# Kernel optimization log

Measured on AMD Instinct MI355X. Metric: run time of the kernel, lower is better.

Reference implementation:

```python
import jax, jax.numpy as jnp
import numpy as np
from jax import lax

D_MODEL = 768
EXPAND = 2
D_INNER = D_MODEL * EXPAND  # 1536
N_STATE = 16
DT_RANK = D_INNER // 16  # 96
K_CONV = 4
B, L = 2, 1024


def setup_inputs() -> dict:
    key = jax.random.key(0)
    ks = jax.random.split(key, 20)
    s = lambda i, shape, scale=0.02: jax.random.normal(ks[i], shape, dtype=jnp.float32) * scale
    # dt_proj bias init (inverse softplus of dt in [0.001, 0.1])
    def dt_bias(k):
        dt = jnp.exp(jax.random.uniform(k, (D_INNER,)) * (np.log(0.1) - np.log(0.001)) + np.log(0.001))
        return dt + jnp.log(-jnp.expm1(-dt))
    A_log = jnp.log(jnp.arange(1, N_STATE + 1, dtype=jnp.float32))[None, :] * jnp.ones((D_INNER, 1), jnp.float32)
    inp = {
        "u": jax.random.normal(ks[0], (B, L, D_MODEL), dtype=jnp.float32),
        "norm_w": jnp.ones((D_MODEL,), jnp.float32),
        "norm_b": jnp.zeros((D_MODEL,), jnp.float32),
        "fwd_in_w": s(1, (2 * D_INNER, D_MODEL)),
        "fwd_conv_w": s(2, (D_INNER, 1, K_CONV), 0.1),
        "fwd_conv_b": jnp.zeros((D_INNER,), jnp.float32),
        "fwd_A_log": A_log,
        "fwd_xproj_w": s(3, (DT_RANK + 2 * N_STATE, D_INNER)),
        "fwd_dt_w": s(4, (D_INNER, DT_RANK)),
        "fwd_dt_b": dt_bias(ks[5]),
        "fwd_D": jnp.ones((D_INNER,), jnp.float32),
        "bwd_in_w": s(6, (2 * D_INNER, D_MODEL)),
        "bwd_conv_w": s(7, (D_INNER, 1, K_CONV), 0.1),
        "bwd_conv_b": jnp.zeros((D_INNER,), jnp.float32),
        "bwd_A_log": A_log,
        "bwd_xproj_w": s(8, (DT_RANK + 2 * N_STATE, D_INNER)),
        "bwd_dt_w": s(9, (D_INNER, DT_RANK)),
        "bwd_dt_b": dt_bias(ks[10]),
        "bwd_D": jnp.ones((D_INNER,), jnp.float32),
        "out_w": s(11, (D_MODEL, 2 * D_INNER)),
    }
    return inp


def _layernorm(x, w, b, eps=1e-5):
    mu = jnp.mean(x, axis=-1, keepdims=True)
    var = jnp.mean(jnp.square(x - mu), axis=-1, keepdims=True)
    return (x - mu) * lax.rsqrt(var + eps) * w + b


def _dw_causal_conv(x, w, b):
    # x: (B, L, D); torch Conv1d(pad=k-1, groups=D) then trim to L == left-pad causal conv
    xc = jnp.transpose(x, (0, 2, 1))  # (B, D, L)
    y = lax.conv_general_dilated(xc, w, window_strides=(1,),
                                 padding=[(K_CONV - 1, 0)],
                                 feature_group_count=D_INNER,
                                 dimension_numbers=('NCH', 'OIH', 'NCH'))
    return jnp.transpose(y + b[None, :, None], (0, 2, 1))


def _ssm(x, A_log, xproj_w, dt_w, dt_b, Dp):
    # x: (B, L, D)
    x_dbl = x @ xproj_w.T  # (B, L, dt_rank + 2N)
    dt_raw = x_dbl[..., :DT_RANK]
    B_sel = x_dbl[..., DT_RANK:DT_RANK + N_STATE]   # (B, L, N)
    C_sel = x_dbl[..., DT_RANK + N_STATE:]           # (B, L, N)
    dt = jax.nn.softplus(dt_raw @ dt_w.T + dt_b)      # (B, L, D)
    A = -jnp.exp(A_log)                               # (D, N)
    A_bar = jnp.exp(dt[..., None] * A)                # (B, L, D, N)
    Bu = (dt * x)[..., None] * B_sel[:, :, None, :]   # (B, L, D, N)
    # linear recurrence h_t = A_bar_t * h_{t-1} + Bu_t via associative scan
    def combine(c1, c2):
        a1, b1 = c1
        a2, b2 = c2
        return a1 * a2, a2 * b1 + b2
    _, h = lax.associative_scan(combine, (A_bar, Bu), axis=1)
    y = jnp.einsum('bldn,bln->bld', h, C_sel)
    return y + x * Dp


def _branch(u, in_w, conv_w, conv_b, A_log, xproj_w, dt_w, dt_b, Dp, reverse):
    if reverse:
        u = u[:, ::-1]
    xz = u @ in_w.T
    x, z = xz[..., :D_INNER], xz[..., D_INNER:]
    x = jax.nn.silu(_dw_causal_conv(x, conv_w, conv_b))
    x = _ssm(x, A_log, xproj_w, dt_w, dt_b, Dp)
    x = x * jax.nn.silu(z)
    if reverse:
        x = x[:, ::-1]
    return x


def reference(u, norm_w, norm_b,
              fwd_in_w, fwd_conv_w, fwd_conv_b, fwd_A_log, fwd_xproj_w, fwd_dt_w, fwd_dt_b, fwd_D,
              bwd_in_w, bwd_conv_w, bwd_conv_b, bwd_A_log, bwd_xproj_w, bwd_dt_w, bwd_dt_b, bwd_D,
              out_w):
    residual = u
    un = _layernorm(u, norm_w, norm_b)
    x_fwd = _branch(un, fwd_in_w, fwd_conv_w, fwd_conv_b, fwd_A_log, fwd_xproj_w, fwd_dt_w, fwd_dt_b, fwd_D, False)
    x_bwd = _branch(un, bwd_in_w, bwd_conv_w, bwd_conv_b, bwd_A_log, bwd_xproj_w, bwd_dt_w, bwd_dt_b, bwd_D, True)
    x = jnp.concatenate([x_fwd, x_bwd], axis=-1) @ out_w.T
    return x + residual
```

## Files before the change

kernel.cpp:

```cpp
#include <hip/hip_runtime.h>
#include <hip/hip_bf16.h>

#define D_MODEL 768
#define D_INNER 1536
#define N_STATE 16
#define DT_RANK 96
#define KCONV   4
#define Bv      2
#define Lv      1024
#define MROWS   (Bv*Lv)
#define CH      128
#define G       (Lv/CH)
#define PADL    68

typedef __attribute__((ext_vector_type(8))) short bf16x8;
typedef __attribute__((ext_vector_type(4))) float f32x4;

__device__ __forceinline__ void gll16(const void* g, void* l) {
    __builtin_amdgcn_global_load_lds(
        (const __attribute__((address_space(1))) void*)g,
        (__attribute__((address_space(3))) void*)l, 16, 0, 0);
}

__device__ __forceinline__ unsigned short f2bf(float f) {
    unsigned u = __builtin_bit_cast(unsigned, f);
    u += 0x7fffu + ((u >> 16) & 1u);
    return (unsigned short)(u >> 16);
}

template<int CTRL>
__device__ __forceinline__ float dpp_ror_add(float v) {
    int vi = __builtin_bit_cast(int, v);
    int mv = __builtin_amdgcn_update_dpp(vi, vi, CTRL, 0xf, 0xf, true);
    return v + __builtin_bit_cast(float, mv);
}

__global__ __launch_bounds__(256)
void ln_kernel(const float* __restrict__ u, const float* __restrict__ w,
               const float* __restrict__ bvec, unsigned short* __restrict__ o)
{
    int row = blockIdx.x;
    const float* x = u + (size_t)row * D_MODEL;
    int t = threadIdx.x;
    float v0 = x[t], v1 = x[t + 256], v2 = x[t + 512];
    float s  = v0 + v1 + v2;
    float s2 = v0*v0 + v1*v1 + v2*v2;
    for (int off = 32; off; off >>= 1) {
        s  += __shfl_down(s, off);
        s2 += __shfl_down(s2, off);
    }
    __shared__ float rs[4], rs2[4];
    __shared__ float mu_s, rstd_s;
    int wid = t >> 6, lane = t & 63;
    if (lane == 0) { rs[wid] = s; rs2[wid] = s2; }
    __syncthreads();
    if (t == 0) {
        float S  = rs[0] + rs[1] + rs[2] + rs[3];
        float S2 = rs2[0] + rs2[1] + rs2[2] + rs2[3];
        float mu = S / (float)D_MODEL;
        float var = S2 / (float)D_MODEL - mu * mu;
        mu_s = mu;
        rstd_s = rsqrtf(var + 1e-5f);
    }
    __syncthreads();
    float mu = mu_s, r = rstd_s;
    unsigned short* orow = o + (size_t)row * D_MODEL;
    orow[t]       = f2bf((v0 - mu) * r * w[t]       + bvec[t]);
    orow[t + 256] = f2bf((v1 - mu) * r * w[t + 256] + bvec[t + 256]);
    orow[t + 512] = f2bf((v2 - mu) * r * w[t + 512] + bvec[t + 512]);
}

__global__ __launch_bounds__(256)
void f2b(const float* __restrict__ in, unsigned short* __restrict__ o, int n4)
{
    int i = blockIdx.x * 256 + threadIdx.x;
    if (i < n4) {
        float4 v = ((const float4*)in)[i];
        ushort4 r;
        r.x = f2bf(v.x); r.y = f2bf(v.y); r.z = f2bf(v.z); r.w = f2bf(v.w);
        ((ushort4*)o)[i] = r;
    }
}

__global__ __launch_bounds__(256)
void gemm_mfma(const unsigned short* __restrict__ A, int lda, int revA, int Lr,
               const unsigned short* __restrict__ W,
               const float* __restrict__ bias, int act,
               const float* __restrict__ res,
               float* __restrict__ C,
               int M, int N, int K)
{
    __shared__ unsigned short As[128 * 32];
    __shared__ unsigned short Bs[128 * 32];
    const int tid = threadIdx.x;
    const int m0 = blockIdx.y * 128, n0 = blockIdx.x * 128;
    const int lane = tid & 63;
    const int w  = tid >> 6;
    const int wr = w >> 1, wc = w & 1;
    const int lm = lane & 15, lk = lane >> 4;

    const int srow = tid >> 2;
    const int skq  = (tid & 3) * 8;
    int arow0 = m0 + srow, arow1 = m0 + srow + 64;
    if (revA) {
        arow0 = (arow0 / Lr) * Lr + (Lr - 1 - arow0 % Lr);
        arow1 = (arow1 / Lr) * Lr + (Lr - 1 - arow1 % Lr);
    }
    const unsigned short* a0 = A + (size_t)arow0 * lda + skq;
    const unsigned short* a1 = A + (size_t)arow1 * lda + skq;
    const unsigned short* w0 = W + (size_t)(n0 + srow) * K + skq;
    const unsigned short* w1 = W + (size_t)(n0 + srow + 64) * K + skq;

    f32x4 acc[4][4] = {};

    for (int k0 = 0; k0 < K; k0 += 32) {
        __syncthreads();
        gll16(a0 + k0, &As[tid * 8]);
        gll16(a1 + k0, &As[2048 + tid * 8]);
        gll16(w0 + k0, &Bs[tid * 8]);
        gll16(w1 + k0, &Bs[2048 + tid * 8]);
        __syncthreads();

        bf16x8 af[4], bfr[4];
        #pragma unroll
        for (int i = 0; i < 4; i++) {
            af[i]  = *(const bf16x8*)&As[(wr * 64 + i * 16 + lm) * 32 + lk * 8];
            bfr[i] = *(const bf16x8*)&Bs[(wc * 64 + i * 16 + lm) * 32 + lk * 8];
        }
        #pragma unroll
        for (int i = 0; i < 4; i++)
            #pragma unroll
            for (int j = 0; j < 4; j++)
                acc[i][j] = __builtin_amdgcn_mfma_f32_16x16x32_bf16(af[i], bfr[j], acc[i][j], 0, 0, 0);
    }

    #pragma unroll
    for (int i = 0; i < 4; i++) {
        #pragma unroll
        for (int j = 0; j < 4; j++) {
            int row = m0 + wr * 64 + i * 16 + lk * 4;
            int col = n0 + wc * 64 + j * 16 + lm;
            #pragma unroll
            for (int r = 0; r < 4; r++) {
                float v = acc[i][j][r];
                if (bias) v += bias[col];
                if (act == 2) v = (v > 20.f) ? v : log1pf(__expf(v));
                if (res)  v += res[(size_t)(row + r) * N + col];
                C[(size_t)(row + r) * N + col] = v;
            }
        }
    }
}

__global__ __launch_bounds__(256)
void conv_silu(const float* __restrict__ xz, const float* __restrict__ w,
               const float* __restrict__ bias, float* __restrict__ xo,
               unsigned short* __restrict__ xbf)
{
    int t  = blockIdx.x * 256 + threadIdx.x;
    int d  = t % D_INNER;
    int lc = (t / D_INNER) % (Lv / 8);
    int b  = t / (D_INNER * (Lv / 8));
    int l0 = lc * 8;
    const float* src = xz + (size_t)b * Lv * (2 * D_INNER) + d;
    float w0 = w[d*4], w1 = w[d*4+1], w2 = w[d*4+2], w3 = w[d*4+3];
    float bb = bias[d];
    float v[11];
    #pragma unroll
    for (int j = 0; j < 11; j++) {
        int l = l0 - 3 + j;
        v[j] = (l >= 0) ? src[(size_t)l * (2 * D_INNER)] : 0.f;
    }
    size_t base = ((size_t)b * Lv + l0) * D_INNER + d;
    #pragma unroll
    for (int j = 0; j < 8; j++) {
        float a = bb + w0*v[j] + w1*v[j+1] + w2*v[j+2] + w3*v[j+3];
        a = a / (1.f + __expf(-a));
        xo[base + (size_t)j * D_INNER] = a;
        xbf[base + (size_t)j * D_INNER] = f2bf(a);
    }
}

__global__ __launch_bounds__(128, 6)
void scan1(const float* __restrict__ xF, const float* __restrict__ dtF,
           const float* __restrict__ xdF, const float* __restrict__ AlF,
           const float* __restrict__ xB, const float* __restrict__ dtB,
           const float* __restrict__ xdB, const float* __restrict__ AlB,
           float* __restrict__ h_end, float* __restrict__ Send)
{
    const int br = blockIdx.z;
    const int bb = blockIdx.y >> 3, g = blockIdx.y & 7;
    const int d0 = blockIdx.x * 8;

    const float* x    = br ? xB  : xF;
    const float* dt   = br ? dtB : dtF;
    const float* xd   = br ? xdB : xdF;
    const float* Alog = br ? AlB : AlF;

    __shared__ float xs [2][8][PADL];
    __shared__ float dls[2][8][PADL];
    __shared__ float Bss[2][16][PADL];

    const int t = threadIdx.x;
    const int n = t & 15, dloc = t >> 4;

    const float* xg  = x  + ((size_t)bb * Lv + g * CH) * D_INNER + d0;
    const float* dtg = dt + ((size_t)bb * Lv + g * CH) * D_INNER + d0;
    const float* bcg = xd + ((size_t)bb * Lv + g * CH) * 128;

    const int sl = t >> 1, sdq = (t & 1) * 4;
    const int bl0 = t >> 2,         bq0 = (t & 3) * 4;
    const int bl1 = (t + 128) >> 2, bq1 = ((t + 128) & 3) * 4;

    f32x4 rx, rdt, rb0, rb1;

    #define LOADG1(c) do {                                                       \
        int l0_ = (c) * 64;                                                      \
        rx  = *(const f32x4*)(xg  + (size_t)(l0_ + sl) * D_INNER + sdq);         \
        rdt = *(const f32x4*)(dtg + (size_t)(l0_ + sl) * D_INNER + sdq);         \
        rb0 = *(const f32x4*)(bcg + (size_t)(l0_ + bl0) * 128 + DT_RANK + bq0);  \
        rb1 = *(const f32x4*)(bcg + (size_t)(l0_ + bl1) * 128 + DT_RANK + bq1);  \
    } while (0)

    #define WRITEL1(p) do {                                                     \
        _Pragma("unroll")                                                       \
        for (int j = 0; j < 4; j++) {                                           \
            xs [p][sdq+j][sl] = rx[j];                                          \
            dls[p][sdq+j][sl] = rdt[j];                                         \
            Bss[p][bq0+j][bl0] = rb0[j];                                        \
            Bss[p][bq1+j][bl1] = rb1[j];                                        \
        }                                                                       \
    } while (0)

    const float An = -__expf(Alog[(d0 + dloc) * N_STATE + n]);
    float h = 0.f, srun = 0.f;

    LOADG1(0);
    WRITEL1(0);
    __syncthreads();

    for (int c = 0; c < 2; ++c) {
        const int p = c;
        if (c == 0) LOADG1(1);

        #pragma unroll
        for (int gg = 0; gg < 16; ++gg) {
            f32x4 xv  = *(const f32x4*)&xs [p][dloc][gg*4];
            f32x4 dtv = *(const f32x4*)&dls[p][dloc][gg*4];
            f32x4 bv  = *(const f32x4*)&Bss[p][n][gg*4];
            #pragma unroll
            for (int j = 0; j < 4; ++j) {
                float ab = __expf(dtv[j] * An);
                h = fmaf(ab, h, dtv[j] * xv[j] * bv[j]);
                srun += dtv[j];
            }
        }
        if (c == 0) { WRITEL1(1); }
        __syncthreads();
    }
    h_end[(((size_t)(br*Bv + bb) * G + g) * D_INNER + d0 + dloc) * 16 + n] = h;
    if (n == 0)
        Send[((size_t)(br*Bv + bb) * G + g) * D_INNER + d0 + dloc] = srun;
    #undef LOADG1
    #undef WRITEL1
}

__global__ __launch_bounds__(256)
void scan2(const float* __restrict__ Send,
           const float* __restrict__ AlF, const float* __restrict__ AlB,
           const float* __restrict__ h_end, float* __restrict__ h0buf)
{
    int idx = blockIdx.x * 256 + threadIdx.x;
    int n = idx & 15;
    int rest = idx >> 4;
    int d  = rest % D_INNER;
    int bbr = rest / D_INNER;
    int bb = bbr & 1, br = bbr >> 1;

    const float* Alog = br ? AlB : AlF;
    float An = -__expf(Alog[d * N_STATE + n]);

    float h0 = 0.f;
    #pragma unroll
    for (int g = 0; g < G; ++g) {
        size_t base = (((size_t)(br*Bv + bb) * G + g) * D_INNER + d) * 16 + n;
        h0buf[base] = h0;
        float Se = Send[((size_t)(br*Bv + bb) * G + g) * D_INNER + d];
        h0 = __expf(An * Se) * h0 + h_end[base];
    }
}

__global__ __launch_bounds__(128, 4)
void scan3(const float* __restrict__ xF, const float* __restrict__ dtF,
           const float* __restrict__ xdF, const float* __restrict__ xzF,
           const float* __restrict__ AlF, const float* __restrict__ DFp,
           const float* __restrict__ xB, const float* __restrict__ dtB,
           const float* __restrict__ xdB, const float* __restrict__ xzB,
           const float* __restrict__ AlB, const float* __restrict__ DBp,
           const float* __restrict__ h0buf, unsigned short* __restrict__ ycat)
{
    const int br = blockIdx.z;
    const int bb = blockIdx.y >> 3, g = blockIdx.y & 7;
    const int d0 = blockIdx.x * 8;

    const float* x    = br ? xB  : xF;
    const float* dt   = br ? dtB : dtF;
    const float* xd   = br ? xdB : xdF;
    const float* xz   = br ? xzB : xzF;
    const float* Alog = br ? AlB : AlF;
    const float* Dp   = br ? DBp : DFp;

    __shared__ float xs [2][8][PADL];
    __shared__ float dls[2][8][PADL];
    __shared__ float zs [2][8][PADL];
    __shared__ float Bss[2][16][PADL];
    __shared__ float Css[2][16][PADL];

    const int t = threadIdx.x;
    const int n = t & 15, dloc = t >> 4;

    const float* xg  = x  + ((size_t)bb * Lv + g * CH) * D_INNER + d0;
    const float* dtg = dt + ((size_t)bb * Lv + g * CH) * D_INNER + d0;
    const float* zg  = xz + ((size_t)bb * Lv + g * CH) * (2*D_INNER) + D_INNER + d0;
    const float* bcg = xd + ((size_t)bb * Lv + g * CH) * 128;

    const int sl = t >> 1, sdq = (t & 1) * 4;
    const int bl0 = t >> 2,         bq0 = (t & 3) * 4;
    const int bl1 = (t + 128) >> 2, bq1 = ((t + 128) & 3) * 4;

    f32x4 rx, rdt, rz, rb0, rb1, rc0, rc1;

    #define LOADG3(c) do {                                                       \
        int l0_ = (c) * 64;                                                      \
        rx  = *(const f32x4*)(xg  + (size_t)(l0_ + sl) * D_INNER + sdq);         \
        rdt = *(const f32x4*)(dtg + (size_t)(l0_ + sl) * D_INNER + sdq);         \
        rz  = *(const f32x4*)(zg  + (size_t)(l0_ + sl) * (2*D_INNER) + sdq);     \
        rb0 = *(const f32x4*)(bcg + (size_t)(l0_ + bl0) * 128 + DT_RANK           + bq0); \
        rb1 = *(const f32x4*)(bcg + (size_t)(l0_ + bl1) * 128 + DT_RANK           + bq1); \
        rc0 = *(const f32x4*)(bcg + (size_t)(l0_ + bl0) * 128 + DT_RANK + N_STATE + bq0); \
        rc1 = *(const f32x4*)(bcg + (size_t)(l0_ + bl1) * 128 + DT_RANK + N_STATE + bq1); \
    } while (0)

    #define WRITEL3(p) do {                                                     \
        _Pragma("unroll")                                                       \
        for (int j = 0; j < 4; j++) {                                           \
            xs [p][sdq+j][sl] = rx[j];                                          \
            dls[p][sdq+j][sl] = rdt[j];                                         \
            zs [p][sdq+j][sl] = rz[j];                                          \
            Bss[p][bq0+j][bl0] = rb0[j];                                        \
            Bss[p][bq1+j][bl1] = rb1[j];                                        \
            Css[p][bq0+j][bl0] = rc0[j];                                        \
            Css[p][bq1+j][bl1] = rc1[j];                                        \
        }                                                                       \
    } while (0)

    const float An = -__expf(Alog[(d0 + dloc) * N_STATE + n]);
    const float Dd = Dp[d0 + dloc];
    float h = h0buf[(((size_t)(br*Bv + bb) * G + g) * D_INNER + d0 + dloc) * 16 + n];

    LOADG3(0);
    WRITEL3(0);
    __syncthreads();

    for (int c = 0; c < 2; ++c) {
        const int p = c;
        if (c == 0) LOADG3(1);

        float yq[4] = {};
        #pragma unroll
        for (int gg = 0; gg < 16; ++gg) {
            f32x4 xv  = *(const f32x4*)&xs [p][dloc][gg*4];
            f32x4 dtv = *(const f32x4*)&dls[p][dloc][gg*4];
            f32x4 zv  = *(const f32x4*)&zs [p][dloc][gg*4];
            f32x4 bv  = *(const f32x4*)&Bss[p][n][gg*4];
            f32x4 cv  = *(const f32x4*)&Css[p][n][gg*4];
            #pragma unroll
            for (int j = 0; j < 4; ++j) {
                const int l = gg * 4 + j;
                float ab = __expf(dtv[j] * An);
                h = fmaf(ab, h, dtv[j] * xv[j] * bv[j]);
                float contrib = h * cv[j];
                contrib = dpp_ror_add<0x121>(contrib);
                contrib = dpp_ror_add<0x122>(contrib);
                contrib = dpp_ror_add<0x124>(contrib);
                contrib = dpp_ror_add<0x128>(contrib);
                float y = (contrib + xv[j] * Dd)
                        * (zv[j] * __builtin_amdgcn_rcpf(1.f + __expf(-zv[j])));
                if ((l & 15) == n) yq[l >> 4] = y;
            }
        }
        if (c == 0) { WRITEL3(1); }

        #pragma unroll
        for (int q = 0; q < 4; ++q) {
            int gl = g * CH + c * 64 + q * 16 + n;
            int lo = br ? (Lv - 1 - gl) : gl;
            ycat[((size_t)bb * Lv + lo) * (2*D_INNER) + br * D_INNER + d0 + dloc] = f2bf(yq[q]);
        }
        __syncthreads();
    }
    #undef LOADG3
    #undef WRITEL3
}

extern "C" void kernel_launch(void* const* d_in, const int* in_sizes, int n_in,
                              void* d_out, int out_size, void* d_ws, size_t ws_size,
                              hipStream_t stream)
{
    (void)in_sizes; (void)n_in; (void)out_size; (void)ws_size;
    const float* u        = (const float*)d_in[0];
    const float* norm_w   = (const float*)d_in[1];
    const float* norm_b   = (const float*)d_in[2];
    const float* f_in_w   = (const float*)d_in[3];
    const float* f_conv_w = (const float*)d_in[4];
    const float* f_conv_b = (const float*)d_in[5];
    const float* f_Alog   = (const float*)d_in[6];
    const float* f_xproj  = (const float*)d_in[7];
    const float* f_dt_w   = (const float*)d_in[8];
    const float* f_dt_b   = (const float*)d_in[9];
    const float* f_D      = (const float*)d_in[10];
    const float* b_in_w   = (const float*)d_in[11];
    const float* b_conv_w = (const float*)d_in[12];
    const float* b_conv_b = (const float*)d_in[13];
    const float* b_Alog   = (const float*)d_in[14];
    const float* b_xproj  = (const float*)d_in[15];
    const float* b_dt_w   = (const float*)d_in[16];
    const float* b_dt_b   = (const float*)d_in[17];
    const float* b_D      = (const float*)d_in[18];
    const float* out_w    = (const float*)d_in[19];
    float* out = (float*)d_out;

    float* p = (float*)d_ws;
    unsigned short* un_bf = (unsigned short*)p;  p += (size_t)MROWS * D_MODEL;
    float* xz_f   = p;  p += (size_t)MROWS * 2 * D_INNER;
    float* xz_b   = p;  p += (size_t)MROWS * 2 * D_INNER;
    float* x_f    = p;  p += (size_t)MROWS * D_INNER;
    float* x_b    = p;  p += (size_t)MROWS * D_INNER;
    unsigned short* xbf_f = (unsigned short*)p;  p += (size_t)MROWS * D_INNER / 2;
    unsigned short* xbf_b = (unsigned short*)p;  p += (size_t)MROWS * D_INNER / 2;
    float* xdbl_f = p;  p += (size_t)MROWS * 128;
    float* xdbl_b = p;  p += (size_t)MROWS * 128;
    float* dt_f   = p;  p += (size_t)MROWS * D_INNER;
    float* dt_b_  = p;  p += (size_t)MROWS * D_INNER;
    unsigned short* yc_bf = (unsigned short*)p;  p += (size_t)MROWS * D_INNER;
    unsigned short* fw_bf = (unsigned short*)p;  p += (size_t)D_INNER * D_MODEL;
    unsigned short* bw_bf = (unsigned short*)p;  p += (size_t)D_INNER * D_MODEL;
    unsigned short* xwf_bf = (unsigned short*)p; p += (size_t)64 * D_INNER;
    unsigned short* xwb_bf = (unsigned short*)p; p += (size_t)64 * D_INNER;
    unsigned short* ow_bf = (unsigned short*)p;  p += (size_t)D_MODEL * D_INNER;
    float* h_end  = p;  p += (size_t)2 * Bv * G * D_INNER * N_STATE;
    float* h0buf  = p;  p += (size_t)2 * Bv * G * D_INNER * N_STATE;
    float* Send   = p;  p += (size_t)2 * Bv * G * D_INNER;
    unsigned short* xdbf_f = (unsigned short*)p; p += (size_t)MROWS * 128 / 2;
    unsigned short* xdbf_b = (unsigned short*)p; p += (size_t)MROWS * 128 / 2;
    unsigned short* dtwf_bf = (unsigned short*)p; p += (size_t)D_INNER * DT_RANK / 2;
    unsigned short* dtwb_bf = (unsigned short*)p; p += (size_t)D_INNER * DT_RANK / 2;

    ln_kernel<<<MROWS, 256, 0, stream>>>(u, norm_w, norm_b, un_bf);

    f2b<<<(2*D_INNER*D_MODEL/4 + 255)/256, 256, 0, stream>>>(f_in_w, fw_bf, 2*D_INNER*D_MODEL/4);
    f2b<<<(2*D_INNER*D_MODEL/4 + 255)/256, 256, 0, stream>>>(b_in_w, bw_bf, 2*D_INNER*D_MODEL/4);
    f2b<<<(128*D_INNER/4 + 255)/256, 256, 0, stream>>>(f_xproj, xwf_bf, 128*D_INNER/4);
    f2b<<<(128*D_INNER/4 + 255)/256, 256, 0, stream>>>(b_xproj, xwb_bf, 128*D_INNER/4);
    f2b<<<(D_MODEL*2*D_INNER/4 + 255)/256, 256, 0, stream>>>(out_w, ow_bf, D_MODEL*2*D_INNER/4);
    f2b<<<(D_INNER*DT_RANK/4 + 255)/256, 256, 0, stream>>>(f_dt_w, dtwf_bf, D_INNER*DT_RANK/4);
    f2b<<<(D_INNER*DT_RANK/4 + 255)/256, 256, 0, stream>>>(b_dt_w, dtwb_bf, D_INNER*DT_RANK/4);

    gemm_mfma<<<dim3(2*D_INNER/128, MROWS/128), 256, 0, stream>>>(
        un_bf, D_MODEL, 0, Lv, fw_bf, nullptr, 0, nullptr, xz_f, MROWS, 2*D_INNER, D_MODEL);
    gemm_mfma<<<dim3(2*D_INNER/128, MROWS/128), 256, 0, stream>>>(
        un_bf, D_MODEL, 1, Lv, bw_bf, nullptr, 0, nullptr, xz_b, MROWS, 2*D_INNER, D_MODEL);

    int convBlocks = (Bv * (Lv/8) * D_INNER) / 256;
    conv_silu<<<convBlocks, 256, 0, stream>>>(xz_f, f_conv_w, f_conv_b, x_f, xbf_f);
    conv_silu<<<convBlocks, 256, 0, stream>>>(xz_b, b_conv_w, b_conv_b, x_b, xbf_b);

    gemm_mfma<<<dim3(1, MROWS/128), 256, 0, stream>>>(
        xbf_f, D_INNER, 0, Lv, xwf_bf, nullptr, 0, nullptr, xdbl_f, MROWS, 128, D_INNER);
    gemm_mfma<<<dim3(1, MROWS/128), 256, 0, stream>>>(
        xbf_b, D_INNER, 0, Lv, xwb_bf, nullptr, 0, nullptr, xdbl_b, MROWS, 128, D_INNER);

    f2b<<<(MROWS*128/4 + 255)/256, 256, 0, stream>>>(xdbl_f, xdbf_f, MROWS*128/4);
    f2b<<<(MROWS*128/4 + 255)/256, 256, 0, stream>>>(xdbl_b, xdbf_b, MROWS*128/4);
    gemm_mfma<<<dim3(D_INNER/128, MROWS/128), 256, 0, stream>>>(
        xdbf_f, 128, 0, Lv, dtwf_bf, f_dt_b, 2, nullptr, dt_f, MROWS, D_INNER, DT_RANK);
    gemm_mfma<<<dim3(D_INNER/128, MROWS/128), 256, 0, stream>>>(
        xdbf_b, 128, 0, Lv, dtwb_bf, b_dt_b, 2, nullptr, dt_b_, MROWS, D_INNER, DT_RANK);

    scan1<<<dim3(D_INNER/8, Bv*G, 2), 128, 0, stream>>>(
        x_f, dt_f, xdbl_f, f_Alog,
        x_b, dt_b_, xdbl_b, b_Alog, h_end, Send);
    scan2<<<(2*Bv*D_INNER*N_STATE)/256, 256, 0, stream>>>(
        Send, f_Alog, b_Alog, h_end, h0buf);
    scan3<<<dim3(D_INNER/8, Bv*G, 2), 128, 0, stream>>>(
        x_f, dt_f, xdbl_f, xz_f, f_Alog, f_D,
        x_b, dt_b_, xdbl_b, xz_b, b_Alog, b_D, h0buf, yc_bf);

    gemm_mfma<<<dim3(D_MODEL/128, MROWS/128), 256, 0, stream>>>(
        yc_bf, 2*D_INNER, 0, Lv, ow_bf, nullptr, 0, u, out, MROWS, D_MODEL, 2*D_INNER);
}
```

Baseline: 570.8 us.

## Split in-proj output, fuse silu(z) into GEMM epilogue, use bf16 x/z in scans

The in-projection GEMM epilogue now writes the x half as fp32 and the z half as bf16 with silu already applied. The conv kernel then reads a compact x buffer and no longer writes an fp32 copy. Both scan kernels read x and silu(z) as bf16 from the existing bf16 buffers and keep them in smaller shared-memory arrays. This cuts global memory traffic and scan shared-memory footprint (scan1 occupancy hint raised to 7), at the cost of bf16 rounding of x and z inside the recurrence.

Measured after the change: 610.5 us. 1.07x slower.

```diff
diff --git a/kernel.cpp b/kernel.cpp
--- a/kernel.cpp
+++ b/kernel.cpp
@@ -26,6 +26,9 @@
     unsigned u = __builtin_bit_cast(unsigned, f);
     u += 0x7fffu + ((u >> 16) & 1u);
     return (unsigned short)(u >> 16);
+}
+__device__ __forceinline__ float b2f(unsigned short s) {
+    return __builtin_bit_cast(float, (unsigned)s << 16);
 }
 
 template<int CTRL>
@@ -87,7 +90,7 @@
                const unsigned short* __restrict__ W,
                const float* __restrict__ bias, int act,
                const float* __restrict__ res,
-               float* __restrict__ C,
+               float* __restrict__ C, unsigned short* __restrict__ Cz,
                int M, int N, int K)
 {
     __shared__ unsigned short As[128 * 32];
@@ -143,48 +146,55 @@
             #pragma unroll
             for (int r = 0; r < 4; r++) {
                 float v = acc[i][j][r];
-                if (bias) v += bias[col];
-                if (act == 2) v = (v > 20.f) ? v : log1pf(__expf(v));
-                if (res)  v += res[(size_t)(row + r) * N + col];
-                C[(size_t)(row + r) * N + col] = v;
+                if (act == 3) {
+                    if (col < D_INNER) {
+                        C[(size_t)(row + r) * D_INNER + col] = v;
+                    } else {
+                        float sv = v * __builtin_amdgcn_rcpf(1.f + __expf(-v));
+                        Cz[(size_t)(row + r) * D_INNER + (col - D_INNER)] = f2bf(sv);
+                    }
+                } else {
+                    if (bias) v += bias[col];
+                    if (act == 2) v = (v > 20.f) ? v : log1pf(__expf(v));
+                    if (res)  v += res[(size_t)(row + r) * N + col];
+                    C[(size_t)(row + r) * N + col] = v;
+                }
             }
         }
     }
 }
 
 __global__ __launch_bounds__(256)
-void conv_silu(const float* __restrict__ xz, const float* __restrict__ w,
-               const float* __restrict__ bias, float* __restrict__ xo,
-               unsigned short* __restrict__ xbf)
+void conv_silu(const float* __restrict__ xzx, const float* __restrict__ w,
+               const float* __restrict__ bias, unsigned short* __restrict__ xbf)
 {
     int t  = blockIdx.x * 256 + threadIdx.x;
     int d  = t % D_INNER;
     int lc = (t / D_INNER) % (Lv / 8);
     int b  = t / (D_INNER * (Lv / 8));
     int l0 = lc * 8;
-    const float* src = xz + (size_t)b * Lv * (2 * D_INNER) + d;
+    const float* src = xzx + (size_t)b * Lv * D_INNER + d;
     float w0 = w[d*4], w1 = w[d*4+1], w2 = w[d*4+2], w3 = w[d*4+3];
     float bb = bias[d];
     float v[11];
     #pragma unroll
     for (int j = 0; j < 11; j++) {
         int l = l0 - 3 + j;
-        v[j] = (l >= 0) ? src[(size_t)l * (2 * D_INNER)] : 0.f;
+        v[j] = (l >= 0) ? src[(size_t)l * D_INNER] : 0.f;
     }
     size_t base = ((size_t)b * Lv + l0) * D_INNER + d;
     #pragma unroll
     for (int j = 0; j < 8; j++) {
         float a = bb + w0*v[j] + w1*v[j+1] + w2*v[j+2] + w3*v[j+3];
         a = a / (1.f + __expf(-a));
-        xo[base + (size_t)j * D_INNER] = a;
         xbf[base + (size_t)j * D_INNER] = f2bf(a);
     }
 }
 
-__global__ __launch_bounds__(128, 6)
-void scan1(const float* __restrict__ xF, const float* __restrict__ dtF,
+__global__ __launch_bounds__(128, 7)
+void scan1(const unsigned short* __restrict__ xF, const float* __restrict__ dtF,
            const float* __restrict__ xdF, const float* __restrict__ AlF,
-           const float* __restrict__ xB, const float* __restrict__ dtB,
+           const unsigned short* __restrict__ xB, const float* __restrict__ dtB,
            const float* __restrict__ xdB, const float* __restrict__ AlB,
            float* __restrict__ h_end, float* __restrict__ Send)
 {
@@ -192,19 +202,19 @@
     const int bb = blockIdx.y >> 3, g = blockIdx.y & 7;
     const int d0 = blockIdx.x * 8;
 
-    const float* x    = br ? xB  : xF;
+    const unsigned short* x = br ? xB  : xF;
     const float* dt   = br ? dtB : dtF;
     const float* xd   = br ? xdB : xdF;
     const float* Alog = br ? AlB : AlF;
 
-    __shared__ float xs [2][8][PADL];
+    __shared__ unsigned short xsh[2][8][PADL];
     __shared__ float dls[2][8][PADL];
     __shared__ float Bss[2][16][PADL];
 
     const int t = threadIdx.x;
     const int n = t & 15, dloc = t >> 4;
 
-    const float* xg  = x  + ((size_t)bb * Lv + g * CH) * D_INNER + d0;
+    const unsigned short* xg = x + ((size_t)bb * Lv + g * CH) * D_INNER + d0;
     const float* dtg = dt + ((size_t)bb * Lv + g * CH) * D_INNER + d0;
     const float* bcg = xd + ((size_t)bb * Lv + g * CH) * 128;
 
@@ -212,20 +222,21 @@
     const int bl0 = t >> 2,         bq0 = (t & 3) * 4;
     const int bl1 = (t + 128) >> 2, bq1 = ((t + 128) & 3) * 4;
 
-    f32x4 rx, rdt, rb0, rb1;
+    ushort4 rxu; f32x4 rdt, rb0, rb1;
 
     #define LOADG1(c) do {                                                       \
         int l0_ = (c) * 64;                                                      \
-        rx  = *(const f32x4*)(xg  + (size_t)(l0_ + sl) * D_INNER + sdq);         \
+        rxu = *(const ushort4*)(xg + (size_t)(l0_ + sl) * D_INNER + sdq);        \
         rdt = *(const f32x4*)(dtg + (size_t)(l0_ + sl) * D_INNER + sdq);         \
         rb0 = *(const f32x4*)(bcg + (size_t)(l0_ + bl0) * 128 + DT_RANK + bq0);  \
         rb1 = *(const f32x4*)(bcg + (size_t)(l0_ + bl1) * 128 + DT_RANK + bq1);  \
     } while (0)
 
     #define WRITEL1(p) do {                                                     \
+        xsh[p][sdq+0][sl] = rxu.x; xsh[p][sdq+1][sl] = rxu.y;                   \
+        xsh[p][sdq+2][sl] = rxu.z; xsh[p][sdq+3][sl] = rxu.w;                   \
         _Pragma("unroll")                                                       \
         for (int j = 0; j < 4; j++) {                                           \
-            xs [p][sdq+j][sl] = rx[j];                                          \
             dls[p][sdq+j][sl] = rdt[j];                                         \
             Bss[p][bq0+j][bl0] = rb0[j];                                        \
             Bss[p][bq1+j][bl1] = rb1[j];                                        \
@@ -245,13 +256,14 @@
 
         #pragma unroll
         for (int gg = 0; gg < 16; ++gg) {
-            f32x4 xv  = *(const f32x4*)&xs [p][dloc][gg*4];
+            ushort4 xv4 = *(const ushort4*)&xsh[p][dloc][gg*4];
             f32x4 dtv = *(const f32x4*)&dls[p][dloc][gg*4];
             f32x4 bv  = *(const f32x4*)&Bss[p][n][gg*4];
+            float xf[4] = { b2f(xv4.x), b2f(xv4.y), b2f(xv4.z), b2f(xv4.w) };
             #pragma unroll
             for (int j = 0; j < 4; ++j) {
                 float ab = __expf(dtv[j] * An);
-                h = fmaf(ab, h, dtv[j] * xv[j] * bv[j]);
+                h = fmaf(ab, h, dtv[j] * xf[j] * bv[j]);
                 srun += dtv[j];
             }
         }
@@ -291,11 +303,11 @@
 }
 
 __global__ __launch_bounds__(128, 4)
-void scan3(const float* __restrict__ xF, const float* __restrict__ dtF,
-           const float* __restrict__ xdF, const float* __restrict__ xzF,
+void scan3(const unsigned short* __restrict__ xF, const float* __restrict__ dtF,
+           const float* __restrict__ xdF, const unsigned short* __restrict__ zF,
            const float* __restrict__ AlF, const float* __restrict__ DFp,
-           const float* __restrict__ xB, const float* __restrict__ dtB,
-           const float* __restrict__ xdB, const float* __restrict__ xzB,
+           const unsigned short* __restrict__ xB, const float* __restrict__ dtB,
+           const float* __restrict__ xdB, const unsigned short* __restrict__ zB,
            const float* __restrict__ AlB, const float* __restrict__ DBp,
            const float* __restrict__ h0buf, unsigned short* __restrict__ ycat)
 {
@@ -303,38 +315,38 @@
     const int bb = blockIdx.y >> 3, g = blockIdx.y & 7;
     const int d0 = blockIdx.x * 8;
 
-    const float* x    = br ? xB  : xF;
+    const unsigned short* x = br ? xB : xF;
     const float* dt   = br ? dtB : dtF;
     const float* xd   = br ? xdB : xdF;
-    const float* xz   = br ? xzB : xzF;
+    const unsigned short* z = br ? zB : zF;
     const float* Alog = br ? AlB : AlF;
     const float* Dp   = br ? DBp : DFp;
 
-    __shared__ float xs [2][8][PADL];
+    __shared__ unsigned short xsh[2][8][PADL];
     __shared__ float dls[2][8][PADL];
-    __shared__ float zs [2][8][PADL];
+    __shared__ unsigned short zsh[2][8][PADL];
     __shared__ float Bss[2][16][PADL];
     __shared__ float Css[2][16][PADL];
 
     const int t = threadIdx.x;
     const int n = t & 15, dloc = t >> 4;
 
-    const float* xg  = x  + ((size_t)bb * Lv + g * CH) * D_INNER + d0;
+    const unsigned short* xg = x + ((size_t)bb * Lv + g * CH) * D_INNER + d0;
     const float* dtg = dt + ((size_t)bb * Lv + g * CH) * D_INNER + d0;
-    const float* zg  = xz + ((size_t)bb * Lv + g * CH) * (2*D_INNER) + D_INNER + d0;
+    const unsigned short* zg = z + ((size_t)bb * Lv + g * CH) * D_INNER + d0;
     const float* bcg = xd + ((size_t)bb * Lv + g * CH) * 128;
 
     const int sl = t >> 1, sdq = (t & 1) * 4;
     const int bl0 = t >> 2,         bq0 = (t & 3) * 4;
     const int bl1 = (t + 128) >> 2, bq1 = ((t + 128) & 3) * 4;
 
-    f32x4 rx, rdt, rz, rb0, rb1, rc0, rc1;
+    ushort4 rxu, rzu; f32x4 rdt, rb0, rb1, rc0, rc1;
 
     #define LOADG3(c) do {                                                       \
         int l0_ = (c) * 64;                                                      \
-        rx  = *(const f32x4*)(xg  + (size_t)(l0_ + sl) * D_INNER + sdq);         \
+        rxu = *(const ushort4*)(xg + (size_t)(l0_ + sl) * D_INNER + sdq);        \
         rdt = *(const f32x4*)(dtg + (size_t)(l0_ + sl) * D_INNER + sdq);         \
-        rz  = *(const f32x4*)(zg  + (size_t)(l0_ + sl) * (2*D_INNER) + sdq);     \
+        rzu = *(const ushort4*)(zg + (size_t)(l0_ + sl) * D_INNER + sdq);        \
         rb0 = *(const f32x4*)(bcg + (size_t)(l0_ + bl0) * 128 + DT_RANK           + bq0); \
         rb1 = *(const f32x4*)(bcg + (size_t)(l0_ + bl1) * 128 + DT_RANK           + bq1); \
         rc0 = *(const f32x4*)(bcg + (size_t)(l0_ + bl0) * 128 + DT_RANK + N_STATE + bq0); \
@@ -342,11 +354,13 @@
     } while (0)
 
     #define WRITEL3(p) do {                                                     \
+        xsh[p][sdq+0][sl] = rxu.x; xsh[p][sdq+1][sl] = rxu.y;                   \
+        xsh[p][sdq+2][sl] = rxu.z; xsh[p][sdq+3][sl] = rxu.w;                   \
+        zsh[p][sdq+0][sl] = rzu.x; zsh[p][sdq+1][sl] = rzu.y;                   \
+        zsh[p][sdq+2][sl] = rzu.z; zsh[p][sdq+3][sl] = rzu.w;                   \
         _Pragma("unroll")                                                       \
         for (int j = 0; j < 4; j++) {                                           \
-            xs [p][sdq+j][sl] = rx[j];                                          \
             dls[p][sdq+j][sl] = rdt[j];                                         \
-            zs [p][sdq+j][sl] = rz[j];                                          \
             Bss[p][bq0+j][bl0] = rb0[j];                                        \
             Bss[p][bq1+j][bl1] = rb1[j];                                        \
             Css[p][bq0+j][bl0] = rc0[j];                                        \
@@ -369,23 +383,24 @@
         float yq[4] = {};
         #pragma unroll
         for (int gg = 0; gg < 16; ++gg) {
-            f32x4 xv  = *(const f32x4*)&xs [p][dloc][gg*4];
+            ushort4 xv4 = *(const ushort4*)&xsh[p][dloc][gg*4];
             f32x4 dtv = *(const f32x4*)&dls[p][dloc][gg*4];
-            f32x4 zv  = *(const f32x4*)&zs [p][dloc][gg*4];
+            ushort4 zv4 = *(const ushort4*)&zsh[p][dloc][gg*4];
             f32x4 bv  = *(const f32x4*)&Bss[p][n][gg*4];
             f32x4 cv  = *(const f32x4*)&Css[p][n][gg*4];
+            float xf[4] = { b2f(xv4.x), b2f(xv4.y), b2f(xv4.z), b2f(xv4.w) };
+            float zf[4] = { b2f(zv4.x), b2f(zv4.y), b2f(zv4.z), b2f(zv4.w) };
             #pragma unroll
             for (int j = 0; j < 4; ++j) {
                 const int l = gg * 4 + j;
                 float ab = __expf(dtv[j] * An);
-                h = fmaf(ab, h, dtv[j] * xv[j] * bv[j]);
+                h = fmaf(ab, h, dtv[j] * xf[j] * bv[j]);
                 float contrib = h * cv[j];
                 contrib = dpp_ror_add<0x121>(contrib);
                 contrib = dpp_ror_add<0x122>(contrib);
                 contrib = dpp_ror_add<0x124>(contrib);
                 contrib = dpp_ror_add<0x128>(contrib);
-                float y = (contrib + xv[j] * Dd)
-                        * (zv[j] * __builtin_amdgcn_rcpf(1.f + __expf(-zv[j])));
+                float y = (contrib + xf[j] * Dd) * zf[j];
                 if ((l & 15) == n) yq[l >> 4] = y;
             }
         }
@@ -432,10 +447,10 @@
 
     float* p = (float*)d_ws;
     unsigned short* un_bf = (unsigned short*)p;  p += (size_t)MROWS * D_MODEL;
-    float* xz_f   = p;  p += (size_t)MROWS * 2 * D_INNER;
-    float* xz_b   = p;  p += (size_t)MROWS * 2 * D_INNER;
-    float* x_f    = p;  p += (size_t)MROWS * D_INNER;
-    float* x_b    = p;  p += (size_t)MROWS * D_INNER;
+    float* xzx_f  = p;  p += (size_t)MROWS * D_INNER;
+    float* xzx_b  = p;  p += (size_t)MROWS * D_INNER;
+    unsigned short* zbf_f = (unsigned short*)p;  p += (size_t)MROWS * D_INNER / 2;
+    unsigned short* zbf_b = (unsigned short*)p;  p += (size_t)MROWS * D_INNER / 2;
     unsigned short* xbf_f = (unsigned short*)p;  p += (size_t)MROWS * D_INNER / 2;
     unsigned short* xbf_b = (unsigned short*)p;  p += (size_t)MROWS * D_INNER / 2;
     float* xdbl_f = p;  p += (size_t)MROWS * 128;
@@ -467,35 +482,35 @@
     f2b<<<(D_INNER*DT_RANK/4 + 255)/256, 256, 0, stream>>>(b_dt_w, dtwb_bf, D_INNER*DT_RANK/4);
 
     gemm_mfma<<<dim3(2*D_INNER/128, MROWS/128), 256, 0, stream>>>(
-        un_bf, D_MODEL, 0, Lv, fw_bf, nullptr, 0, nullptr, xz_f, MROWS, 2*D_INNER, D_MODEL);
+        un_bf, D_MODEL, 0, Lv, fw_bf, nullptr, 3, nullptr, xzx_f, zbf_f, MROWS, 2*D_INNER, D_MODEL);
     gemm_mfma<<<dim3(2*D_INNER/128, MROWS/128), 256, 0, stream>>>(
-        un_bf, D_MODEL, 1, Lv, bw_bf, nullptr, 0, nullptr, xz_b, MROWS, 2*D_INNER, D_MODEL);
+        un_bf, D_MODEL, 1, Lv, bw_bf, nullptr, 3, nullptr, xzx_b, zbf_b, MROWS, 2*D_INNER, D_MODEL);
 
     int convBlocks = (Bv * (Lv/8) * D_INNER) / 256;
-    conv_silu<<<convBlocks, 256, 0, stream>>>(xz_f, f_conv_w, f_conv_b, x_f, xbf_f);
-    conv_silu<<<convBlocks, 256, 0, stream>>>(xz_b, b_conv_w, b_conv_b, x_b, xbf_b);
+    conv_silu<<<convBlocks, 256, 0, stream>>>(xzx_f, f_conv_w, f_conv_b, xbf_f);
+    conv_silu<<<convBlocks, 256, 0, stream>>>(xzx_b, b_conv_w, b_conv_b, xbf_b);
 
     gemm_mfma<<<dim3(1, MROWS/128), 256, 0, stream>>>(
-        xbf_f, D_INNER, 0, Lv, xwf_bf, nullptr, 0, nullptr, xdbl_f, MROWS, 128, D_INNER);
+        xbf_f, D_INNER, 0, Lv, xwf_bf, nullptr, 0, nullptr, xdbl_f, nullptr, MROWS, 128, D_INNER);
     gemm_mfma<<<dim3(1, MROWS/128), 256, 0, stream>>>(
-        xbf_b, D_INNER, 0, Lv, xwb_bf, nullptr, 0, nullptr, xdbl_b, MROWS, 128, D_INNER);
+        xbf_b, D_INNER, 0, Lv, xwb_bf, nullptr, 0, nullptr, xdbl_b, nullptr, MROWS, 128, D_INNER);
 
     f2b<<<(MROWS*128/4 + 255)/256, 256, 0, stream>>>(xdbl_f, xdbf_f, MROWS*128/4);
     f2b<<<(MROWS*128/4 + 255)/256, 256, 0, stream>>>(xdbl_b, xdbf_b, MROWS*128/4);
     gemm_mfma<<<dim3(D_INNER/128, MROWS/128), 256, 0, stream>>>(
-        xdbf_f, 128, 0, Lv, dtwf_bf, f_dt_b, 2, nullptr, dt_f, MROWS, D_INNER, DT_RANK);
+        xdbf_f, 128, 0, Lv, dtwf_bf, f_dt_b, 2, nullptr, dt_f, nullptr, MROWS, D_INNER, DT_RANK);
     gemm_mfma<<<dim3(D_INNER/128, MROWS/128), 256, 0, stream>>>(
-        xdbf_b, 128, 0, Lv, dtwb_bf, b_dt_b, 2, nullptr, dt_b_, MROWS, D_INNER, DT_RANK);
+        xdbf_b, 128, 0, Lv, dtwb_bf, b_dt_b, 2, nullptr, dt_b_, nullptr, MROWS, D_INNER, DT_RANK);
 
     scan1<<<dim3(D_INNER/8, Bv*G, 2), 128, 0, stream>>>(
-        x_f, dt_f, xdbl_f, f_Alog,
-        x_b, dt_b_, xdbl_b, b_Alog, h_end, Send);
+        xbf_f, dt_f, xdbl_f, f_Alog,
+        xbf_b, dt_b_, xdbl_b, b_Alog, h_end, Send);
     scan2<<<(2*Bv*D_INNER*N_STATE)/256, 256, 0, stream>>>(
         Send, f_Alog, b_Alog, h_end, h0buf);
     scan3<<<dim3(D_INNER/8, Bv*G, 2), 128, 0, stream>>>(
-        x_f, dt_f, xdbl_f, xz_f, f_Alog, f_D,
-        x_b, dt_b_, xdbl_b, xz_b, b_Alog, b_D, h0buf, yc_bf);
+        xbf_f, dt_f, xdbl_f, zbf_f, f_Alog, f_D,
+        xbf_b, dt_b_, xdbl_b, zbf_b, b_Alog, b_D, h0buf, yc_bf);
 
     gemm_mfma<<<dim3(D_MODEL/128, MROWS/128), 256, 0, stream>>>(
-        yc_bf, 2*D_INNER, 0, Lv, ow_bf, nullptr, 0, u, out, MROWS, D_MODEL, 2*D_INNER);
-}
+        yc_bf, 2*D_INNER, 0, Lv, ow_bf, nullptr, 0, u, out, nullptr, MROWS, D_MODEL, 2*D_INNER);
+}
```
